# Kernel optimization log

Measured on AMD Instinct MI355X. Metric: run time of the kernel, lower is better.

Reference implementation:

```python
import jax, jax.numpy as jnp
import numpy as np

N = 100000
E = 1600000
F_IN, F_HID, F_OUT = 128, 32, 2


def setup_inputs() -> dict:
    key = jax.random.key(0)
    k1, k2, k3, k4 = jax.random.split(key, 4)
    x = jax.random.normal(k1, (N, F_IN), dtype=jnp.float32)
    edge_index = jax.random.randint(k2, (2, E), 0, N, dtype=jnp.int64)
    # Glorot-style init like torch_geometric GCNConv
    W1 = jax.random.normal(k3, (F_IN, F_HID), dtype=jnp.float32) * (1.0 / np.sqrt(F_IN))
    b1 = jnp.zeros((F_HID,), dtype=jnp.float32)
    W2 = jax.random.normal(k4, (F_HID, F_OUT), dtype=jnp.float32) * (1.0 / np.sqrt(F_HID))
    b2 = jnp.zeros((F_OUT,), dtype=jnp.float32)
    return {"x": x, "edge_index": edge_index, "W1": W1, "b1": b1, "W2": W2, "b2": b2}


def _gcn_conv(x, row, col, norm, W, b):
    # GCNConv: transform, then normalized aggregate (source -> target), then bias
    h = x @ W                                   # [N, F_out]
    msg = norm[:, None] * h[row]                # gather + scale, [E+N, F_out]
    out = jax.ops.segment_sum(msg, col, num_segments=N)  # scatter-add to targets
    return out + b


def reference(x, edge_index, W1, b1, W2, b2):
    # add self-loops (GCNConv default)
    loops = jnp.arange(N, dtype=edge_index.dtype)
    row = jnp.concatenate([edge_index[0], loops])
    col = jnp.concatenate([edge_index[1], loops])
    # symmetric normalization: deg^{-1/2}[row] * deg^{-1/2}[col], deg = in-degree w/ self-loops
    deg = jax.ops.segment_sum(jnp.ones_like(col, dtype=x.dtype), col, num_segments=N)
    dinv = jnp.where(deg > 0, jax.lax.rsqrt(deg), 0.0)
    norm = dinv[row] * dinv[col]                # [E+N]

    h = _gcn_conv(x, row, col, norm, W1, b1)
    h = jax.nn.relu(h)
    h = _gcn_conv(h, row, col, norm, W2, b2)
    return jax.nn.log_softmax(h, axis=1)
```

## Files before the change

### kernel.cpp

```cpp
#include <hip/hip_runtime.h>
#include <hip/hip_bf16.h>
#include <math.h>
#include <stdint.h>


#define GNN_N 100000
#define GNN_E 1600000
#define NBUCK 391
#define CAP 4608
#define CHB 4096
#define EB 391
#define XPAD 136

typedef float fx2 __attribute__((ext_vector_type(2)));
typedef short short8x __attribute__((ext_vector_type(8)));
typedef float f32x4 __attribute__((ext_vector_type(4)));

__device__ inline uint16_t bf16_bits(float f) {
    uint32_t u = __float_as_uint(f);
    return (uint16_t)((u + 0x7fffu + ((u >> 16) & 1u)) >> 16);
}
__device__ inline uint32_t pack_bf2(float lo, float hi) {
    return (uint32_t)bf16_bits(lo) | ((uint32_t)bf16_bits(hi) << 16);
}

__global__ __launch_bounds__(256) void k_fat(const int* __restrict__ row,
                                             const int* __restrict__ col,
                                             int* __restrict__ bucket_fill,
                                             uint32_t* __restrict__ slab,
                                             const float* __restrict__ x,
                                             const float* __restrict__ W1,
                                             uint32_t* __restrict__ h1b,
                                             int e, int n) {
    __shared__ union {
        struct { int hist[NBUCK]; int base[NBUCK]; } bk;
        struct { uint16_t xs[64 * XPAD]; uint16_t w1t[32 * XPAD]; } mm;
    } u;
    const int tid = threadIdx.x;

    if (blockIdx.x < EB) {
        int* hist = u.bk.hist;
        int* base = u.bk.base;
        const int e0 = blockIdx.x * CHB;
        const int m = min(CHB, e - e0);
        const bool full = (m == CHB);

        for (int i = tid; i < NBUCK; i += 256) hist[i] = 0;

        int cc[16], rr[16], pp[16];
        if (full) {
            const int4* c4 = (const int4*)(col + e0);
            const int4* r4 = (const int4*)(row + e0);
            #pragma unroll
            for (int t = 0; t < 4; ++t) {
                int4 c = c4[tid + t * 256];
                int4 r = r4[tid + t * 256];
                cc[t * 4 + 0] = c.x; cc[t * 4 + 1] = c.y;
                cc[t * 4 + 2] = c.z; cc[t * 4 + 3] = c.w;
                rr[t * 4 + 0] = r.x; rr[t * 4 + 1] = r.y;
                rr[t * 4 + 2] = r.z; rr[t * 4 + 3] = r.w;
            }
            __syncthreads();
            #pragma unroll
            for (int t = 0; t < 16; ++t)
                pp[t] = atomicAdd(&hist[cc[t] >> 8], 1);
        } else {
            __syncthreads();
            #pragma unroll
            for (int t = 0; t < 16; ++t) {
                int i = tid + t * 256;
                if (i < m) {
                    cc[t] = col[e0 + i];
                    rr[t] = row[e0 + i];
                    pp[t] = atomicAdd(&hist[cc[t] >> 8], 1);
                }
            }
        }
        __syncthreads();
        for (int i = tid; i < NBUCK; i += 256) {
            int bb = (i + blockIdx.x * 131) % NBUCK;
            base[bb] = atomicAdd(&bucket_fill[bb], hist[bb]);
        }
        __syncthreads();
        if (full) {
            #pragma unroll
            for (int t = 0; t < 16; ++t) {
                int b = cc[t] >> 8;
                int p = base[b] + pp[t];
                if (p < CAP)
                    slab[(size_t)b * CAP + p] = ((uint32_t)rr[t] << 8) | (uint32_t)(cc[t] & 255);
            }
        } else {
            #pragma unroll
            for (int t = 0; t < 16; ++t) {
                int i = tid + t * 256;
                if (i < m) {
                    int b = cc[t] >> 8;
                    int p = base[b] + pp[t];
                    if (p < CAP)
                        slab[(size_t)b * CAP + p] = ((uint32_t)rr[t] << 8) | (uint32_t)(cc[t] & 255);
                }
            }
        }
    } else {
        uint16_t* xs = u.mm.xs;
        uint16_t* w1t = u.mm.w1t;
        const int nodeBase = (blockIdx.x - EB) * 64;

        for (int i = tid; i < 4096; i += 256) {
            int k = i >> 5, c = i & 31;
            w1t[c * XPAD + k] = bf16_bits(W1[i]);
        }
        {
            const float4* x4 = (const float4*)x;
            for (int i = tid; i < 64 * 32; i += 256) {
                int node = i >> 5;
                int k4 = i & 31;
                float4 v = make_float4(0.f, 0.f, 0.f, 0.f);
                if (nodeBase + node < n)
                    v = x4[(size_t)(nodeBase + node) * 32 + k4];
                int b = node * XPAD + k4 * 4;
                xs[b + 0] = bf16_bits(v.x); xs[b + 1] = bf16_bits(v.y);
                xs[b + 2] = bf16_bits(v.z); xs[b + 3] = bf16_bits(v.w);
            }
        }
        __syncthreads();

        const int wave = tid >> 6;
        const int lane = tid & 63;
        const int nn = lane & 15;
        const int quad = lane >> 4;
        f32x4 acc0 = {0.f, 0.f, 0.f, 0.f};
        f32x4 acc1 = {0.f, 0.f, 0.f, 0.f};
        const int xrow = (wave * 16 + nn) * XPAD;
        #pragma unroll
        for (int s = 0; s < 4; ++s) {
            const int kof = s * 32 + quad * 8;
            short8x bfrag = *(const short8x*)&xs[xrow + kof];
            short8x a0 = *(const short8x*)&w1t[nn * XPAD + kof];
            short8x a1 = *(const short8x*)&w1t[(16 + nn) * XPAD + kof];
            acc0 = __builtin_amdgcn_mfma_f32_16x16x32_bf16(a0, bfrag, acc0, 0, 0, 0);
            acc1 = __builtin_amdgcn_mfma_f32_16x16x32_bf16(a1, bfrag, acc1, 0, 0, 0);
        }
        const int gn = nodeBase + wave * 16 + nn;
        if (gn < n) {
            uint2* h1b2 = (uint2*)h1b;
            h1b2[(size_t)gn * 8 + quad] =
                make_uint2(pack_bf2(acc0[0], acc0[1]), pack_bf2(acc0[2], acc0[3]));
            h1b2[(size_t)gn * 8 + 4 + quad] =
                make_uint2(pack_bf2(acc1[0], acc1[1]), pack_bf2(acc1[2], acc1[3]));
        }
    }
}

__global__ __launch_bounds__(512) void k_fine(uint32_t* __restrict__ slab,
                                              const int* __restrict__ bucket_fill,
                                              const uint32_t* __restrict__ h1b,
                                              uint16_t* __restrict__ h1q16,
                                              uint32_t* __restrict__ offsets,
                                              float* __restrict__ dinv, int n) {
    __shared__ int hist[256];
    __shared__ int excl[256];
    __shared__ int wsum[4];
    __shared__ uint32_t stage[CAP];
    const int tid = threadIdx.x;
    const int b = blockIdx.x;
    const int lane = tid & 63, wave = tid >> 6;

    if (tid < 256) hist[tid] = 0;
    __syncthreads();
    const int nb = min(bucket_fill[b], CAP);
    uint32_t* sl = slab + (size_t)b * CAP;

    uint32_t uu[9];
    int pp[9];
    #pragma unroll
    for (int j = 0; j < 9; ++j) {
        int i = tid + j * 512;
        if (i < nb) {
            uint32_t u = sl[i];
            uu[j] = u;
            pp[j] = atomicAdd(&hist[u & 255u], 1);
        }
    }
    __syncthreads();
    int v = 0, inc = 0;
    if (tid < 256) {
        v = hist[tid];
        inc = v;
        #pragma unroll
        for (int d = 1; d < 64; d <<= 1) {
            int t = __shfl_up(inc, d);
            if (lane >= d) inc += t;
        }
        if (lane == 63) wsum[wave] = inc;
    }
    __syncthreads();
    if (tid == 0) {
        int a = 0;
        #pragma unroll
        for (int w = 0; w < 4; ++w) { int t = wsum[w]; wsum[w] = a; a += t; }
    }
    __syncthreads();
    if (tid < 256) {
        int ex = inc - v + wsum[wave];
        excl[tid] = ex;
        int c = b * 256 + tid;
        if (c < n) {
            offsets[c] = ((uint32_t)min(v, 2047) << 21) | (uint32_t)(b * CAP + ex);
            dinv[c] = rsqrtf((float)(v + 1));
        }
    }
    __syncthreads();
    #pragma unroll
    for (int j = 0; j < 9; ++j) {
        int i = tid + j * 512;
        if (i < nb)
            stage[excl[uu[j] & 255u] + pp[j]] = uu[j] >> 8;
    }
    #pragma unroll
    for (int it = 0; it < 8; ++it) {
        int i = tid + it * 512;
        int node = i >> 4, j = i & 15;
        int c = b * 256 + node;
        if (c < n) {
            float dc = rsqrtf((float)(hist[node] + 1));
            uint32_t w = h1b[(size_t)c * 16 + j];
            float lo = __uint_as_float(w << 16) * dc;
            float hi = __uint_as_float(w & 0xffff0000u) * dc;
            int pk = __builtin_amdgcn_cvt_pk_fp8_f32(lo, hi, 0, false);
            h1q16[(size_t)c * 16 + j] = (uint16_t)pk;
        }
    }
    __syncthreads();
    for (int i = tid; i < nb; i += 512)
        sl[i] = stage[i];
}

__device__ inline void fp8x16_acc(float* a, uint4 u) {
    fx2 p;
    p = __builtin_amdgcn_cvt_pk_f32_fp8(u.x, false); a[0] += p.x;  a[1] += p.y;
    p = __builtin_amdgcn_cvt_pk_f32_fp8(u.x, true);  a[2] += p.x;  a[3] += p.y;
    p = __builtin_amdgcn_cvt_pk_f32_fp8(u.y, false); a[4] += p.x;  a[5] += p.y;
    p = __builtin_amdgcn_cvt_pk_f32_fp8(u.y, true);  a[6] += p.x;  a[7] += p.y;
    p = __builtin_amdgcn_cvt_pk_f32_fp8(u.z, false); a[8] += p.x;  a[9] += p.y;
    p = __builtin_amdgcn_cvt_pk_f32_fp8(u.z, true);  a[10] += p.x; a[11] += p.y;
    p = __builtin_amdgcn_cvt_pk_f32_fp8(u.w, false); a[12] += p.x; a[13] += p.y;
    p = __builtin_amdgcn_cvt_pk_f32_fp8(u.w, true);  a[14] += p.x; a[15] += p.y;
}

__global__ __launch_bounds__(256) void k_gather1(const uint32_t* __restrict__ offsets,
                                                 const uint32_t* __restrict__ sorted,
                                                 const uint32_t* __restrict__ h1q,
                                                 const float* __restrict__ dinv,
                                                 const float* __restrict__ b1,
                                                 const float* __restrict__ W2,
                                                 float* __restrict__ h2s, int n) {
    __shared__ float sb1[32];
    __shared__ float sW2[64];
    const int tid = threadIdx.x;
    if (tid < 32) sb1[tid] = b1[tid];
    else if (tid < 96) sW2[tid - 32] = W2[tid - 32];
    __syncthreads();

    const int l = tid & 1;
    const int node = blockIdx.x * 128 + (tid >> 1);
    if (node >= n) return;
    const uint4* h4 = (const uint4*)h1q;
    float acc[16], acc2[16];
    #pragma unroll
    for (int j = 0; j < 16; ++j) { acc[j] = 0.f; acc2[j] = 0.f; }
    fp8x16_acc(acc, h4[(size_t)node * 2 + l]);
    const uint32_t ow = offsets[node];
    const int start = (int)(ow & 0x1FFFFFu);
    const int deg = (int)(ow >> 21);
    const uint32_t* sr = sorted + start;
    int k = 0;
    for (; k + 8 <= deg; k += 8) {
        int r[8];
        uint4 u[8];
        #pragma unroll
        for (int t = 0; t < 8; ++t) r[t] = (int)sr[k + t];
        #pragma unroll
        for (int t = 0; t < 8; ++t) u[t] = h4[(size_t)r[t] * 2 + l];
        #pragma unroll
        for (int t = 0; t < 8; ++t) fp8x16_acc((t & 1) ? acc2 : acc, u[t]);
    }
    for (; k + 2 <= deg; k += 2) {
        int ra = (int)sr[k], rb = (int)sr[k + 1];
        uint4 ua = h4[(size_t)ra * 2 + l];
        uint4 ub = h4[(size_t)rb * 2 + l];
        fp8x16_acc(acc, ua);
        fp8x16_acc(acc2, ub);
    }
    if (k < deg)
        fp8x16_acc(acc, h4[(size_t)(int)sr[k] * 2 + l]);
    #pragma unroll
    for (int j = 0; j < 16; ++j) acc[j] += acc2[j];

    const float dc = dinv[node];
    const int f0 = l * 16;
    float s0 = 0.f, s1 = 0.f;
    #pragma unroll
    for (int j = 0; j < 16; ++j) {
        float a = fmaxf(dc * acc[j] + sb1[f0 + j], 0.f);
        s0 += a * sW2[(f0 + j) * 2];
        s1 += a * sW2[(f0 + j) * 2 + 1];
    }
    s0 += __shfl_xor(s0, 1);
    s1 += __shfl_xor(s1, 1);
    if (l == 0) ((float2*)h2s)[node] = make_float2(dc * s0, dc * s1);
}

__global__ __launch_bounds__(256) void k_gather2(const uint32_t* __restrict__ offsets,
                                                 const uint32_t* __restrict__ sorted,
                                                 const float* __restrict__ h2s,
                                                 const float* __restrict__ dinv,
                                                 const float* __restrict__ b2,
                                                 float* __restrict__ out, int n) {
    const int tid = threadIdx.x;
    const int l = tid & 3;
    const int node = blockIdx.x * 64 + (tid >> 2);
    if (node >= n) return;
    const float2* h2 = (const float2*)h2s;
    float sx = 0.f, sy = 0.f;
    if (l == 0) { float2 s = h2[node]; sx = s.x; sy = s.y; }
    const uint32_t ow = offsets[node];
    const int start = (int)(ow & 0x1FFFFFu);
    const int deg = (int)(ow >> 21);
    for (int k = l; k < deg; k += 4) {
        float2 v = h2[sorted[start + k]];
        sx += v.x; sy += v.y;
    }
    sx += __shfl_xor(sx, 1); sx += __shfl_xor(sx, 2);
    sy += __shfl_xor(sy, 1); sy += __shfl_xor(sy, 2);
    if (l == 0) {
        float d = dinv[node];
        float v0 = d * sx + b2[0];
        float v1 = d * sy + b2[1];
        float m = fmaxf(v0, v1);
        float lg = m + logf(expf(v0 - m) + expf(v1 - m));
        ((float2*)out)[node] = make_float2(v0 - lg, v1 - lg);
    }
}

extern "C" void kernel_launch(void* const* d_in, const int* in_sizes, int n_in,
                              void* d_out, int out_size, void* d_ws, size_t ws_size,
                              hipStream_t stream) {
    const float* x  = (const float*)d_in[0];
    const int*   ei = (const int*)d_in[1];
    const float* W1 = (const float*)d_in[2];
    const float* b1 = (const float*)d_in[3];
    const float* W2 = (const float*)d_in[4];
    const float* b2 = (const float*)d_in[5];
    float* out = (float*)d_out;
    char* ws = (char*)d_ws;

    const int N = GNN_N, E = GNN_E;
    const int* row = ei;
    const int* col = ei + GNN_E;

    float*    dinv        = (float*)    ws;
    uint32_t* offsets     = (uint32_t*)(ws + 4ull *  100000);
    int*      bucket_fill = (int*)     (ws + 4ull *  200000);
    float*    h2s         = (float*)   (ws + 4ull *  201024);
    uint32_t* h1q         = (uint32_t*)(ws + 4ull *  401024);
    uint32_t* h1b         = (uint32_t*)(ws + 4ull * 1201024);
    uint32_t* slab        = (uint32_t*)(ws + 4ull * 2801024);

    hipMemsetAsync(bucket_fill, 0, 1024 * sizeof(int), stream);

    const int MB = (N + 63) / 64;
    k_fat    <<<EB + MB, 256, 0, stream>>>(row, col, bucket_fill, slab, x, W1, h1b, E, N);
    k_fine   <<<NBUCK, 512, 0, stream>>>(slab, bucket_fill, h1b, (uint16_t*)h1q,
                                         offsets, dinv, N);
    k_gather1<<<(N + 127) / 128, 256, 0, stream>>>(offsets, slab, h1q, dinv, b1, W2, h2s, N);
    k_gather2<<<(N + 63) / 64, 256, 0, stream>>>(offsets, slab, h2s, dinv, b2, out, N);
}
```

Baseline: 166.3 us.

## Fuse four GCN kernels into one persistent kernel with grid barriers

```diff
diff --git a/kernel.cpp b/kernel.cpp
--- a/kernel.cpp
+++ b/kernel.cpp
@@ -9,7 +9,6 @@
 #define NBUCK 391
 #define CAP 4608
 #define CHB 4096
-#define EB 391
 #define XPAD 136
 
 typedef float fx2 __attribute__((ext_vector_type(2)));
@@ -22,219 +21,6 @@
 }
 __device__ inline uint32_t pack_bf2(float lo, float hi) {
     return (uint32_t)bf16_bits(lo) | ((uint32_t)bf16_bits(hi) << 16);
-}
-
-__global__ __launch_bounds__(256) void k_fat(const int* __restrict__ row,
-                                             const int* __restrict__ col,
-                                             int* __restrict__ bucket_fill,
-                                             uint32_t* __restrict__ slab,
-                                             const float* __restrict__ x,
-                                             const float* __restrict__ W1,
-                                             uint32_t* __restrict__ h1b,
-                                             int e, int n) {
-    __shared__ union {
-        struct { int hist[NBUCK]; int base[NBUCK]; } bk;
-        struct { uint16_t xs[64 * XPAD]; uint16_t w1t[32 * XPAD]; } mm;
-    } u;
-    const int tid = threadIdx.x;
-
-    if (blockIdx.x < EB) {
-        int* hist = u.bk.hist;
-        int* base = u.bk.base;
-        const int e0 = blockIdx.x * CHB;
-        const int m = min(CHB, e - e0);
-        const bool full = (m == CHB);
-
-        for (int i = tid; i < NBUCK; i += 256) hist[i] = 0;
-
-        int cc[16], rr[16], pp[16];
-        if (full) {
-            const int4* c4 = (const int4*)(col + e0);
-            const int4* r4 = (const int4*)(row + e0);
-            #pragma unroll
-            for (int t = 0; t < 4; ++t) {
-                int4 c = c4[tid + t * 256];
-                int4 r = r4[tid + t * 256];
-                cc[t * 4 + 0] = c.x; cc[t * 4 + 1] = c.y;
-                cc[t * 4 + 2] = c.z; cc[t * 4 + 3] = c.w;
-                rr[t * 4 + 0] = r.x; rr[t * 4 + 1] = r.y;
-                rr[t * 4 + 2] = r.z; rr[t * 4 + 3] = r.w;
-            }
-            __syncthreads();
-            #pragma unroll
-            for (int t = 0; t < 16; ++t)
-                pp[t] = atomicAdd(&hist[cc[t] >> 8], 1);
-        } else {
-            __syncthreads();
-            #pragma unroll
-            for (int t = 0; t < 16; ++t) {
-                int i = tid + t * 256;
-                if (i < m) {
-                    cc[t] = col[e0 + i];
-                    rr[t] = row[e0 + i];
-                    pp[t] = atomicAdd(&hist[cc[t] >> 8], 1);
-                }
-            }
-        }
-        __syncthreads();
-        for (int i = tid; i < NBUCK; i += 256) {
-            int bb = (i + blockIdx.x * 131) % NBUCK;
-            base[bb] = atomicAdd(&bucket_fill[bb], hist[bb]);
-        }
-        __syncthreads();
-        if (full) {
-            #pragma unroll
-            for (int t = 0; t < 16; ++t) {
-                int b = cc[t] >> 8;
-                int p = base[b] + pp[t];
-                if (p < CAP)
-                    slab[(size_t)b * CAP + p] = ((uint32_t)rr[t] << 8) | (uint32_t)(cc[t] & 255);
-            }
-        } else {
-            #pragma unroll
-            for (int t = 0; t < 16; ++t) {
-                int i = tid + t * 256;
-                if (i < m) {
-                    int b = cc[t] >> 8;
-                    int p = base[b] + pp[t];
-                    if (p < CAP)
-                        slab[(size_t)b * CAP + p] = ((uint32_t)rr[t] << 8) | (uint32_t)(cc[t] & 255);
-                }
-            }
-        }
-    } else {
-        uint16_t* xs = u.mm.xs;
-        uint16_t* w1t = u.mm.w1t;
-        const int nodeBase = (blockIdx.x - EB) * 64;
-
-        for (int i = tid; i < 4096; i += 256) {
-            int k = i >> 5, c = i & 31;
-            w1t[c * XPAD + k] = bf16_bits(W1[i]);
-        }
-        {
-            const float4* x4 = (const float4*)x;
-            for (int i = tid; i < 64 * 32; i += 256) {
-                int node = i >> 5;
-                int k4 = i & 31;
-                float4 v = make_float4(0.f, 0.f, 0.f, 0.f);
-                if (nodeBase + node < n)
-                    v = x4[(size_t)(nodeBase + node) * 32 + k4];
-                int b = node * XPAD + k4 * 4;
-                xs[b + 0] = bf16_bits(v.x); xs[b + 1] = bf16_bits(v.y);
-                xs[b + 2] = bf16_bits(v.z); xs[b + 3] = bf16_bits(v.w);
-            }
-        }
-        __syncthreads();
-
-        const int wave = tid >> 6;
-        const int lane = tid & 63;
-        const int nn = lane & 15;
-        const int quad = lane >> 4;
-        f32x4 acc0 = {0.f, 0.f, 0.f, 0.f};
-        f32x4 acc1 = {0.f, 0.f, 0.f, 0.f};
-        const int xrow = (wave * 16 + nn) * XPAD;
-        #pragma unroll
-        for (int s = 0; s < 4; ++s) {
-            const int kof = s * 32 + quad * 8;
-            short8x bfrag = *(const short8x*)&xs[xrow + kof];
-            short8x a0 = *(const short8x*)&w1t[nn * XPAD + kof];
-            short8x a1 = *(const short8x*)&w1t[(16 + nn) * XPAD + kof];
-            acc0 = __builtin_amdgcn_mfma_f32_16x16x32_bf16(a0, bfrag, acc0, 0, 0, 0);
-            acc1 = __builtin_amdgcn_mfma_f32_16x16x32_bf16(a1, bfrag, acc1, 0, 0, 0);
-        }
-        const int gn = nodeBase + wave * 16 + nn;
-        if (gn < n) {
-            uint2* h1b2 = (uint2*)h1b;
-            h1b2[(size_t)gn * 8 + quad] =
-                make_uint2(pack_bf2(acc0[0], acc0[1]), pack_bf2(acc0[2], acc0[3]));
-            h1b2[(size_t)gn * 8 + 4 + quad] =
-                make_uint2(pack_bf2(acc1[0], acc1[1]), pack_bf2(acc1[2], acc1[3]));
-        }
-    }
-}
-
-__global__ __launch_bounds__(512) void k_fine(uint32_t* __restrict__ slab,
-                                              const int* __restrict__ bucket_fill,
-                                              const uint32_t* __restrict__ h1b,
-                                              uint16_t* __restrict__ h1q16,
-                                              uint32_t* __restrict__ offsets,
-                                              float* __restrict__ dinv, int n) {
-    __shared__ int hist[256];
-    __shared__ int excl[256];
-    __shared__ int wsum[4];
-    __shared__ uint32_t stage[CAP];
-    const int tid = threadIdx.x;
-    const int b = blockIdx.x;
-    const int lane = tid & 63, wave = tid >> 6;
-
-    if (tid < 256) hist[tid] = 0;
-    __syncthreads();
-    const int nb = min(bucket_fill[b], CAP);
-    uint32_t* sl = slab + (size_t)b * CAP;
-
-    uint32_t uu[9];
-    int pp[9];
-    #pragma unroll
-    for (int j = 0; j < 9; ++j) {
-        int i = tid + j * 512;
-        if (i < nb) {
-            uint32_t u = sl[i];
-            uu[j] = u;
-            pp[j] = atomicAdd(&hist[u & 255u], 1);
-        }
-    }
-    __syncthreads();
-    int v = 0, inc = 0;
-    if (tid < 256) {
-        v = hist[tid];
-        inc = v;
-        #pragma unroll
-        for (int d = 1; d < 64; d <<= 1) {
-            int t = __shfl_up(inc, d);
-            if (lane >= d) inc += t;
-        }
-        if (lane == 63) wsum[wave] = inc;
-    }
-    __syncthreads();
-    if (tid == 0) {
-        int a = 0;
-        #pragma unroll
-        for (int w = 0; w < 4; ++w) { int t = wsum[w]; wsum[w] = a; a += t; }
-    }
-    __syncthreads();
-    if (tid < 256) {
-        int ex = inc - v + wsum[wave];
-        excl[tid] = ex;
-        int c = b * 256 + tid;
-        if (c < n) {
-            offsets[c] = ((uint32_t)min(v, 2047) << 21) | (uint32_t)(b * CAP + ex);
-            dinv[c] = rsqrtf((float)(v + 1));
-        }
-    }
-    __syncthreads();
-    #pragma unroll
-    for (int j = 0; j < 9; ++j) {
-        int i = tid + j * 512;
-        if (i < nb)
-            stage[excl[uu[j] & 255u] + pp[j]] = uu[j] >> 8;
-    }
-    #pragma unroll
-    for (int it = 0; it < 8; ++it) {
-        int i = tid + it * 512;
-        int node = i >> 4, j = i & 15;
-        int c = b * 256 + node;
-        if (c < n) {
-            float dc = rsqrtf((float)(hist[node] + 1));
-            uint32_t w = h1b[(size_t)c * 16 + j];
-            float lo = __uint_as_float(w << 16) * dc;
-            float hi = __uint_as_float(w & 0xffff0000u) * dc;
-            int pk = __builtin_amdgcn_cvt_pk_fp8_f32(lo, hi, 0, false);
-            h1q16[(size_t)c * 16 + j] = (uint16_t)pk;
-        }
-    }
-    __syncthreads();
-    for (int i = tid; i < nb; i += 512)
-        sl[i] = stage[i];
 }
 
 __device__ inline void fp8x16_acc(float* a, uint4 u) {
@@ -249,98 +35,306 @@
     p = __builtin_amdgcn_cvt_pk_f32_fp8(u.w, true);  a[14] += p.x; a[15] += p.y;
 }
 
-__global__ __launch_bounds__(256) void k_gather1(const uint32_t* __restrict__ offsets,
-                                                 const uint32_t* __restrict__ sorted,
-                                                 const uint32_t* __restrict__ h1q,
-                                                 const float* __restrict__ dinv,
+__device__ inline void grid_bar(int* bar, int nblk) {
+    __syncthreads();
+    if (threadIdx.x == 0) {
+        __threadfence();
+        int prev = __hip_atomic_fetch_add(bar, 1, __ATOMIC_ACQ_REL,
+                                          __HIP_MEMORY_SCOPE_AGENT);
+        if (prev + 1 < nblk) {
+            while (__hip_atomic_load(bar, __ATOMIC_ACQUIRE,
+                                     __HIP_MEMORY_SCOPE_AGENT) < nblk)
+                __builtin_amdgcn_s_sleep(16);
+        }
+        __threadfence();
+    }
+    __syncthreads();
+}
+
+__global__ __launch_bounds__(512, 4) void k_mega(const int* __restrict__ row,
+                                                 const int* __restrict__ col,
+                                                 int* __restrict__ bucket_fill,
+                                                 int* __restrict__ bars,
+                                                 uint32_t* __restrict__ slab,
+                                                 const float* __restrict__ x,
+                                                 const float* __restrict__ W1,
                                                  const float* __restrict__ b1,
                                                  const float* __restrict__ W2,
-                                                 float* __restrict__ h2s, int n) {
-    __shared__ float sb1[32];
-    __shared__ float sW2[64];
+                                                 const float* __restrict__ b2,
+                                                 uint32_t* __restrict__ h1q,
+                                                 float* __restrict__ h2s,
+                                                 float* __restrict__ out,
+                                                 int e, int n) {
+    __shared__ union {
+        struct { int hist[NBUCK]; int base[NBUCK]; } bk;
+        struct { uint16_t xs[128 * XPAD]; uint16_t w1t[32 * XPAD]; } mm;
+        struct { int hist[256]; int excl[256]; int wsum[4];
+                 uint32_t stage[CAP]; float sb1[32]; float sW2[64]; } fi;
+    } u;
+    __shared__ uint32_t h1l[256 * 16];
     const int tid = threadIdx.x;
-    if (tid < 32) sb1[tid] = b1[tid];
-    else if (tid < 96) sW2[tid - 32] = W2[tid - 32];
-    __syncthreads();
-
-    const int l = tid & 1;
-    const int node = blockIdx.x * 128 + (tid >> 1);
-    if (node >= n) return;
-    const uint4* h4 = (const uint4*)h1q;
-    float acc[16], acc2[16];
-    #pragma unroll
-    for (int j = 0; j < 16; ++j) { acc[j] = 0.f; acc2[j] = 0.f; }
-    fp8x16_acc(acc, h4[(size_t)node * 2 + l]);
-    const uint32_t ow = offsets[node];
-    const int start = (int)(ow & 0x1FFFFFu);
-    const int deg = (int)(ow >> 21);
-    const uint32_t* sr = sorted + start;
-    int k = 0;
-    for (; k + 8 <= deg; k += 8) {
-        int r[8];
-        uint4 u[8];
-        #pragma unroll
-        for (int t = 0; t < 8; ++t) r[t] = (int)sr[k + t];
-        #pragma unroll
-        for (int t = 0; t < 8; ++t) u[t] = h4[(size_t)r[t] * 2 + l];
-        #pragma unroll
-        for (int t = 0; t < 8; ++t) fp8x16_acc((t & 1) ? acc2 : acc, u[t]);
-    }
-    for (; k + 2 <= deg; k += 2) {
-        int ra = (int)sr[k], rb = (int)sr[k + 1];
-        uint4 ua = h4[(size_t)ra * 2 + l];
-        uint4 ub = h4[(size_t)rb * 2 + l];
-        fp8x16_acc(acc, ua);
-        fp8x16_acc(acc2, ub);
-    }
-    if (k < deg)
-        fp8x16_acc(acc, h4[(size_t)(int)sr[k] * 2 + l]);
-    #pragma unroll
-    for (int j = 0; j < 16; ++j) acc[j] += acc2[j];
-
-    const float dc = dinv[node];
-    const int f0 = l * 16;
-    float s0 = 0.f, s1 = 0.f;
-    #pragma unroll
-    for (int j = 0; j < 16; ++j) {
-        float a = fmaxf(dc * acc[j] + sb1[f0 + j], 0.f);
-        s0 += a * sW2[(f0 + j) * 2];
-        s1 += a * sW2[(f0 + j) * 2 + 1];
-    }
-    s0 += __shfl_xor(s0, 1);
-    s1 += __shfl_xor(s1, 1);
-    if (l == 0) ((float2*)h2s)[node] = make_float2(dc * s0, dc * s1);
-}
-
-__global__ __launch_bounds__(256) void k_gather2(const uint32_t* __restrict__ offsets,
-                                                 const uint32_t* __restrict__ sorted,
-                                                 const float* __restrict__ h2s,
-                                                 const float* __restrict__ dinv,
-                                                 const float* __restrict__ b2,
-                                                 float* __restrict__ out, int n) {
-    const int tid = threadIdx.x;
-    const int l = tid & 3;
-    const int node = blockIdx.x * 64 + (tid >> 2);
-    if (node >= n) return;
-    const float2* h2 = (const float2*)h2s;
-    float sx = 0.f, sy = 0.f;
-    if (l == 0) { float2 s = h2[node]; sx = s.x; sy = s.y; }
-    const uint32_t ow = offsets[node];
-    const int start = (int)(ow & 0x1FFFFFu);
-    const int deg = (int)(ow >> 21);
-    for (int k = l; k < deg; k += 4) {
-        float2 v = h2[sorted[start + k]];
-        sx += v.x; sy += v.y;
-    }
-    sx += __shfl_xor(sx, 1); sx += __shfl_xor(sx, 2);
-    sy += __shfl_xor(sy, 1); sy += __shfl_xor(sy, 2);
-    if (l == 0) {
-        float d = dinv[node];
-        float v0 = d * sx + b2[0];
-        float v1 = d * sy + b2[1];
-        float m = fmaxf(v0, v1);
-        float lg = m + logf(expf(v0 - m) + expf(v1 - m));
-        ((float2*)out)[node] = make_float2(v0 - lg, v1 - lg);
+    const int b = blockIdx.x;
+    const int lane = tid & 63, wave = tid >> 6;
+    uint32_t* sl = slab + (size_t)b * CAP;
+
+    {
+        int* hist = u.bk.hist;
+        int* base = u.bk.base;
+        const int e0 = b * CHB;
+        const int m = min(CHB, e - e0);
+        const bool full = (m == CHB);
+
+        for (int i = tid; i < NBUCK; i += 512) hist[i] = 0;
+
+        int cc[8], rr[8], pp[8];
+        if (full) {
+            const int4* c4 = (const int4*)(col + e0);
+            const int4* r4 = (const int4*)(row + e0);
+            #pragma unroll
+            for (int t = 0; t < 2; ++t) {
+                int4 c = c4[tid + t * 512];
+                int4 r = r4[tid + t * 512];
+                cc[t * 4 + 0] = c.x; cc[t * 4 + 1] = c.y;
+                cc[t * 4 + 2] = c.z; cc[t * 4 + 3] = c.w;
+                rr[t * 4 + 0] = r.x; rr[t * 4 + 1] = r.y;
+                rr[t * 4 + 2] = r.z; rr[t * 4 + 3] = r.w;
+            }
+            __syncthreads();
+            #pragma unroll
+            for (int t = 0; t < 8; ++t)
+                pp[t] = atomicAdd(&hist[cc[t] >> 8], 1);
+        } else {
+            __syncthreads();
+            #pragma unroll
+            for (int t = 0; t < 8; ++t) {
+                int i = tid + t * 512;
+                if (i < m) {
+                    cc[t] = col[e0 + i];
+                    rr[t] = row[e0 + i];
+                    pp[t] = atomicAdd(&hist[cc[t] >> 8], 1);
+                }
+            }
+        }
+        __syncthreads();
+        for (int i = tid; i < NBUCK; i += 512) {
+            int bb = (i + b * 131) % NBUCK;
+            base[bb] = atomicAdd(&bucket_fill[bb], hist[bb]);
+        }
+        __syncthreads();
+        if (full) {
+            #pragma unroll
+            for (int t = 0; t < 8; ++t) {
+                int bb = cc[t] >> 8;
+                int p = base[bb] + pp[t];
+                if (p < CAP)
+                    slab[(size_t)bb * CAP + p] = ((uint32_t)rr[t] << 8) | (uint32_t)(cc[t] & 255);
+            }
+        } else {
+            #pragma unroll
+            for (int t = 0; t < 8; ++t) {
+                int i = tid + t * 512;
+                if (i < m) {
+                    int bb = cc[t] >> 8;
+                    int p = base[bb] + pp[t];
+                    if (p < CAP)
+                        slab[(size_t)bb * CAP + p] = ((uint32_t)rr[t] << 8) | (uint32_t)(cc[t] & 255);
+                }
+            }
+        }
+        __syncthreads();
+    }
+
+    {
+        uint16_t* xs = u.mm.xs;
+        uint16_t* w1t = u.mm.w1t;
+        for (int i = tid; i < 4096; i += 512) {
+            int k = i >> 5, c = i & 31;
+            w1t[c * XPAD + k] = bf16_bits(W1[i]);
+        }
+        const float4* x4 = (const float4*)x;
+        #pragma unroll
+        for (int g = 0; g < 2; ++g) {
+            const int nodeBase = b * 256 + g * 128;
+            for (int i = tid; i < 128 * 32; i += 512) {
+                int node = i >> 5;
+                int k4 = i & 31;
+                float4 v = make_float4(0.f, 0.f, 0.f, 0.f);
+                if (nodeBase + node < n)
+                    v = x4[(size_t)(nodeBase + node) * 32 + k4];
+                int bo = node * XPAD + k4 * 4;
+                xs[bo + 0] = bf16_bits(v.x); xs[bo + 1] = bf16_bits(v.y);
+                xs[bo + 2] = bf16_bits(v.z); xs[bo + 3] = bf16_bits(v.w);
+            }
+            __syncthreads();
+            const int nn = lane & 15;
+            const int quad = lane >> 4;
+            f32x4 acc0 = {0.f, 0.f, 0.f, 0.f};
+            f32x4 acc1 = {0.f, 0.f, 0.f, 0.f};
+            const int xrow = (wave * 16 + nn) * XPAD;
+            #pragma unroll
+            for (int s = 0; s < 4; ++s) {
+                const int kof = s * 32 + quad * 8;
+                short8x bfrag = *(const short8x*)&xs[xrow + kof];
+                short8x a0 = *(const short8x*)&w1t[nn * XPAD + kof];
+                short8x a1 = *(const short8x*)&w1t[(16 + nn) * XPAD + kof];
+                acc0 = __builtin_amdgcn_mfma_f32_16x16x32_bf16(a0, bfrag, acc0, 0, 0, 0);
+                acc1 = __builtin_amdgcn_mfma_f32_16x16x32_bf16(a1, bfrag, acc1, 0, 0, 0);
+            }
+            const int nl = g * 128 + wave * 16 + nn;
+            h1l[nl * 16 + 2 * quad + 0] = pack_bf2(acc0[0], acc0[1]);
+            h1l[nl * 16 + 2 * quad + 1] = pack_bf2(acc0[2], acc0[3]);
+            h1l[nl * 16 + 8 + 2 * quad + 0] = pack_bf2(acc1[0], acc1[1]);
+            h1l[nl * 16 + 8 + 2 * quad + 1] = pack_bf2(acc1[2], acc1[3]);
+            __syncthreads();
+        }
+    }
+
+    grid_bar(&bars[0], NBUCK);
+
+    {
+        if (tid < 256) u.fi.hist[tid] = 0;
+        else if (tid < 288) u.fi.sb1[tid - 256] = b1[tid - 256];
+        else if (tid < 352) u.fi.sW2[tid - 288] = W2[tid - 288];
+        __syncthreads();
+        const int nb = min(bucket_fill[b], CAP);
+
+        uint32_t uu[9];
+        int pp[9];
+        #pragma unroll
+        for (int j = 0; j < 9; ++j) {
+            int i = tid + j * 512;
+            if (i < nb) {
+                uint32_t w = sl[i];
+                uu[j] = w;
+                pp[j] = atomicAdd(&u.fi.hist[w & 255u], 1);
+            }
+        }
+        __syncthreads();
+        int v = 0, inc = 0;
+        if (tid < 256) {
+            v = u.fi.hist[tid];
+            inc = v;
+            #pragma unroll
+            for (int d = 1; d < 64; d <<= 1) {
+                int t = __shfl_up(inc, d);
+                if (lane >= d) inc += t;
+            }
+            if (lane == 63) u.fi.wsum[wave] = inc;
+        }
+        __syncthreads();
+        if (tid == 0) {
+            int a = 0;
+            #pragma unroll
+            for (int w = 0; w < 4; ++w) { int t = u.fi.wsum[w]; u.fi.wsum[w] = a; a += t; }
+        }
+        __syncthreads();
+        if (tid < 256) u.fi.excl[tid] = inc - v + u.fi.wsum[wave];
+        __syncthreads();
+        #pragma unroll
+        for (int j = 0; j < 9; ++j) {
+            int i = tid + j * 512;
+            if (i < nb)
+                u.fi.stage[u.fi.excl[uu[j] & 255u] + pp[j]] = uu[j] >> 8;
+        }
+        uint16_t* h1q16 = (uint16_t*)h1q;
+        #pragma unroll
+        for (int it = 0; it < 8; ++it) {
+            int i = tid + it * 512;
+            int node = i >> 4, j = i & 15;
+            int c = b * 256 + node;
+            if (c < n) {
+                float dc = rsqrtf((float)(u.fi.hist[node] + 1));
+                uint32_t w = h1l[node * 16 + j];
+                float lo = __uint_as_float(w << 16) * dc;
+                float hi = __uint_as_float(w & 0xffff0000u) * dc;
+                int pk = __builtin_amdgcn_cvt_pk_fp8_f32(lo, hi, 0, false);
+                h1q16[(size_t)c * 16 + j] = (uint16_t)pk;
+            }
+        }
+    }
+
+    grid_bar(&bars[1], NBUCK);
+
+    {
+        const int l = tid & 1;
+        const int team = tid >> 1;
+        const int c = b * 256 + team;
+        if (c < n) {
+            const uint4* h4 = (const uint4*)h1q;
+            float acc[16], acc2[16];
+            #pragma unroll
+            for (int j = 0; j < 16; ++j) { acc[j] = 0.f; acc2[j] = 0.f; }
+            fp8x16_acc(acc, h4[(size_t)c * 2 + l]);
+            const int ex = u.fi.excl[team];
+            const int deg = u.fi.hist[team];
+            int k = 0;
+            for (; k + 8 <= deg; k += 8) {
+                int r[8];
+                uint4 uv[8];
+                #pragma unroll
+                for (int t = 0; t < 8; ++t) r[t] = (int)u.fi.stage[ex + k + t];
+                #pragma unroll
+                for (int t = 0; t < 8; ++t) uv[t] = h4[(size_t)r[t] * 2 + l];
+                #pragma unroll
+                for (int t = 0; t < 8; ++t) fp8x16_acc((t & 1) ? acc2 : acc, uv[t]);
+            }
+            for (; k + 2 <= deg; k += 2) {
+                uint4 ua = h4[(size_t)(int)u.fi.stage[ex + k] * 2 + l];
+                uint4 ub = h4[(size_t)(int)u.fi.stage[ex + k + 1] * 2 + l];
+                fp8x16_acc(acc, ua);
+                fp8x16_acc(acc2, ub);
+            }
+            if (k < deg)
+                fp8x16_acc(acc, h4[(size_t)(int)u.fi.stage[ex + k] * 2 + l]);
+            #pragma unroll
+            for (int j = 0; j < 16; ++j) acc[j] += acc2[j];
+
+            const float dc = rsqrtf((float)(deg + 1));
+            const int f0 = l * 16;
+            float s0 = 0.f, s1 = 0.f;
+            #pragma unroll
+            for (int j = 0; j < 16; ++j) {
+                float a = fmaxf(dc * acc[j] + u.fi.sb1[f0 + j], 0.f);
+                s0 += a * u.fi.sW2[(f0 + j) * 2];
+                s1 += a * u.fi.sW2[(f0 + j) * 2 + 1];
+            }
+            s0 += __shfl_xor(s0, 1);
+            s1 += __shfl_xor(s1, 1);
+            if (l == 0) ((float2*)h2s)[c] = make_float2(dc * s0, dc * s1);
+        }
+    }
+
+    grid_bar(&bars[2], NBUCK);
+
+    {
+        const float2* h2 = (const float2*)h2s;
+        const int l = tid & 3;
+        const int team = tid >> 2;
+        #pragma unroll
+        for (int it = 0; it < 2; ++it) {
+            const int idx = it * 128 + team;
+            const int c = b * 256 + idx;
+            if (c < n) {
+                float sx = 0.f, sy = 0.f;
+                if (l == 0) { float2 s = h2[c]; sx = s.x; sy = s.y; }
+                const int ex = u.fi.excl[idx];
+                const int deg = u.fi.hist[idx];
+                for (int k = l; k < deg; k += 4) {
+                    float2 v = h2[u.fi.stage[ex + k]];
+                    sx += v.x; sy += v.y;
+                }
+                sx += __shfl_xor(sx, 1); sx += __shfl_xor(sx, 2);
+                sy += __shfl_xor(sy, 1); sy += __shfl_xor(sy, 2);
+                if (l == 0) {
+                    float d = rsqrtf((float)(deg + 1));
+                    float v0 = d * sx + b2[0];
+                    float v1 = d * sy + b2[1];
+                    float m = fmaxf(v0, v1);
+                    float lg = m + logf(expf(v0 - m) + expf(v1 - m));
+                    ((float2*)out)[c] = make_float2(v0 - lg, v1 - lg);
+                }
+            }
+        }
     }
 }
 
@@ -360,20 +354,16 @@
     const int* row = ei;
     const int* col = ei + GNN_E;
 
-    float*    dinv        = (float*)    ws;
-    uint32_t* offsets     = (uint32_t*)(ws + 4ull *  100000);
-    int*      bucket_fill = (int*)     (ws + 4ull *  200000);
-    float*    h2s         = (float*)   (ws + 4ull *  201024);
-    uint32_t* h1q         = (uint32_t*)(ws + 4ull *  401024);
-    uint32_t* h1b         = (uint32_t*)(ws + 4ull * 1201024);
-    uint32_t* slab        = (uint32_t*)(ws + 4ull * 2801024);
-
-    hipMemsetAsync(bucket_fill, 0, 1024 * sizeof(int), stream);
-
-    const int MB = (N + 63) / 64;
-    k_fat    <<<EB + MB, 256, 0, stream>>>(row, col, bucket_fill, slab, x, W1, h1b, E, N);
-    k_fine   <<<NBUCK, 512, 0, stream>>>(slab, bucket_fill, h1b, (uint16_t*)h1q,
-                                         offsets, dinv, N);
-    k_gather1<<<(N + 127) / 128, 256, 0, stream>>>(offsets, slab, h1q, dinv, b1, W2, h2s, N);
-    k_gather2<<<(N + 63) / 64, 256, 0, stream>>>(offsets, slab, h2s, dinv, b2, out, N);
-}
+    int*      bucket_fill = (int*)      ws;
+    int*      bars        = (int*)     (ws + 4ull *    1024);
+    float*    h2s         = (float*)   (ws + 4ull *    1040);
+    uint32_t* h1q         = (uint32_t*)(ws + 4ull *  201040);
+    uint32_t* slab        = (uint32_t*)(ws + 4ull * 1001040);
+
+    hipMemsetAsync(ws, 0, 1040 * sizeof(int), stream);
+
+    int e_arg = E, n_arg = N;
+    k_mega<<<NBUCK, 512, 0, stream>>>(row, col, bucket_fill, bars, slab,
+                                      x, W1, b1, W2, b2, h1q, h2s, out,
+                                      e_arg, n_arg);
+}
```

After: 326.3 us. +96.1%, slower.
